# Kernel tuning notes

Measured on AMD Instinct MI355X. Metric: run time of the kernel, lower is better.

Reference implementation:

```python
import jax, jax.numpy as jnp
import numpy as np

N_HEADS = 8  # SD UNet default for hidden_size=1280
ADAPTER_SCALE = 1.0  # self.scale in SSRAttnProcessor


def setup_inputs() -> dict:
    key = jax.random.key(0)
    ks = jax.random.split(key, 7)
    B, S, D = 16, 4096, 1280
    T, C = 77, 768
    return {
        "hidden_states": jax.random.normal(ks[0], (B, S, D), jnp.float32),
        "encoder_hidden_states": jax.random.normal(ks[1], (B, T, C), jnp.float32),
        "w_q": jax.random.normal(ks[2], (D, D), jnp.float32) * (D ** -0.5),
        "w_k_ssr": jax.random.normal(ks[3], (D, C), jnp.float32) * (C ** -0.5),
        "w_v_ssr": jax.random.normal(ks[4], (D, C), jnp.float32) * (C ** -0.5),
        "w_out": jax.random.normal(ks[5], (D, D), jnp.float32) * (D ** -0.5),
        "b_out": jnp.zeros((D,), jnp.float32),
    }


def reference(hidden_states, encoder_hidden_states, w_q, w_k_ssr, w_v_ssr, w_out, b_out):
    B, S, D = hidden_states.shape
    T = encoder_hidden_states.shape[1]
    H = N_HEADS
    d = D // H
    # projections (torch Linear: x @ W^T)
    q = jnp.einsum('bsc,dc->bsd', hidden_states, w_q)
    k = jnp.einsum('btc,dc->btd', encoder_hidden_states, w_k_ssr)
    v = jnp.einsum('btc,dc->btd', encoder_hidden_states, w_v_ssr)
    # head split: [B, H, S, d]
    q = q.reshape(B, S, H, d).transpose(0, 2, 1, 3)
    k = k.reshape(B, T, H, d).transpose(0, 2, 1, 3)
    v = v.reshape(B, T, H, d).transpose(0, 2, 1, 3)
    # attn.get_attention_scores: softmax(Q K^T * d^-0.5)
    scores = jnp.einsum('bhsd,bhtd->bhst', q, k) * (d ** -0.5)
    probs = jax.nn.softmax(scores, axis=-1)
    out = jnp.einsum('bhst,bhtd->bhsd', probs, v)
    out = out.transpose(0, 2, 1, 3).reshape(B, S, D)
    out = ADAPTER_SCALE * out
    # to_out[0] linear (+ identity dropout); residual_connection=False, rescale=1
    out = jnp.einsum('bsd,ed->bse', out, w_out) + b_out
    return out
```

## Files before the change

### kernel.cpp

```cpp
#include <hip/hip_runtime.h>
#include <hip/hip_bf16.h>

typedef __bf16 bf16x8 __attribute__((ext_vector_type(8)));
typedef short  short8 __attribute__((ext_vector_type(8)));
typedef float  f32x4  __attribute__((ext_vector_type(4)));

__device__ __forceinline__ short f2bs(float f) {
  return __builtin_bit_cast(short, __float2bfloat16(f));
}

__device__ __forceinline__ bf16x8 ldfrag(const short* p) {
  return *reinterpret_cast<const bf16x8*>(p);
}

__global__ __launch_bounds__(256) void cast_f32_bf16(const float* __restrict__ in,
                                                     short* __restrict__ out, int n) {
  int i = (blockIdx.x * 256 + threadIdx.x) * 4;
  if (i < n) {
    float4 v = *reinterpret_cast<const float4*>(in + i);
    out[i + 0] = f2bs(v.x);
    out[i + 1] = f2bs(v.y);
    out[i + 2] = f2bs(v.z);
    out[i + 3] = f2bs(v.w);
  }
}

template <typename AT, typename OT, bool BIAS>
__global__ __launch_bounds__(256)
void gemm_bt(const AT* __restrict__ A, const short* __restrict__ B,
             const float* __restrict__ bias, OT* __restrict__ C,
             int M, int N, int K) {
  __shared__ short As[128][40];
  __shared__ short Bs[128][40];

  const int tid  = threadIdx.x;
  const int wave = tid >> 6, lane = tid & 63;
  const int quad = lane >> 4, l16 = lane & 15;
  const int wy = wave >> 1, wx = wave & 1;
  const int row0 = blockIdx.y * 128, col0 = blockIdx.x * 128;

  const int sr = tid >> 2;
  const int sc = (tid & 3) * 8;

  f32x4 acc[4][4] = {};

  for (int k0 = 0; k0 < K; k0 += 32) {
    for (int p = 0; p < 128; p += 64) {
      const int r  = sr + p;
      const int gm = row0 + r;
      short8 va = {0, 0, 0, 0, 0, 0, 0, 0};
      if (gm < M) {
        if constexpr (sizeof(AT) == 4) {
          const float* ap = (const float*)A + (size_t)gm * K + k0 + sc;
          float4 x = *reinterpret_cast<const float4*>(ap);
          float4 y = *reinterpret_cast<const float4*>(ap + 4);
          va[0] = f2bs(x.x); va[1] = f2bs(x.y); va[2] = f2bs(x.z); va[3] = f2bs(x.w);
          va[4] = f2bs(y.x); va[5] = f2bs(y.y); va[6] = f2bs(y.z); va[7] = f2bs(y.w);
        } else {
          va = *reinterpret_cast<const short8*>((const short*)A + (size_t)gm * K + k0 + sc);
        }
      }
      *reinterpret_cast<short8*>(&As[r][sc]) = va;
      *reinterpret_cast<short8*>(&Bs[r][sc]) =
          *reinterpret_cast<const short8*>(B + (size_t)(col0 + r) * K + k0 + sc);
    }
    __syncthreads();

    bf16x8 af[4], bfv[4];
#pragma unroll
    for (int i = 0; i < 4; i++) af[i]  = ldfrag(&As[wy * 64 + i * 16 + l16][quad * 8]);
#pragma unroll
    for (int i = 0; i < 4; i++) bfv[i] = ldfrag(&Bs[wx * 64 + i * 16 + l16][quad * 8]);
#pragma unroll
    for (int mi = 0; mi < 4; mi++)
#pragma unroll
      for (int ni = 0; ni < 4; ni++)
        acc[mi][ni] = __builtin_amdgcn_mfma_f32_16x16x32_bf16(af[mi], bfv[ni], acc[mi][ni], 0, 0, 0);
    __syncthreads();
  }

#pragma unroll
  for (int mi = 0; mi < 4; mi++) {
#pragma unroll
    for (int r = 0; r < 4; r++) {
      const int row = row0 + wy * 64 + mi * 16 + quad * 4 + r;
      if (row >= M) continue;
#pragma unroll
      for (int ni = 0; ni < 4; ni++) {
        const int col = col0 + wx * 64 + ni * 16 + l16;
        float v = acc[mi][ni][r];
        if constexpr (BIAS) v += bias[col];
        if constexpr (sizeof(OT) == 4)
          C[(size_t)row * N + col] = v;
        else
          C[(size_t)row * N + col] = f2bs(v);
      }
    }
  }
}

__global__ __launch_bounds__(256)
void attn_kernel(const short* __restrict__ Kp, const short* __restrict__ Vp,
                 short* __restrict__ Qb) {
  __shared__ short Vt[160][104];
  __shared__ short Pl[4][16][104];

  const int tid  = threadIdx.x;
  const int b = blockIdx.z, h = blockIdx.y, s0 = blockIdx.x * 64;
  const int wave = tid >> 6, lane = tid & 63;
  const int quad = lane >> 4, l16 = lane & 15;

  for (int idx = tid; idx < 77 * 160; idx += 256) {
    int t = idx / 160, i = idx - t * 160;
    Vt[i][t] = Vp[((size_t)(b * 77 + t)) * 1280 + h * 160 + i];
  }
  for (int idx = tid; idx < 160 * 19; idx += 256) {
    int i = idx / 19, t = 77 + (idx - i * 19);
    Vt[i][t] = 0;
  }
  __syncthreads();

  const short* Qg = Qb + ((size_t)b * 4096 + s0 + wave * 16 + l16) * 1280 + h * 160;
  bf16x8 qf[5];
#pragma unroll
  for (int kc = 0; kc < 5; kc++) qf[kc] = ldfrag(Qg + kc * 32 + quad * 8);

  f32x4 scv[5];
#pragma unroll
  for (int nt = 0; nt < 5; nt++) {
    f32x4 s = {};
    const short* Kg = Kp + ((size_t)(b * 77) + nt * 16 + l16) * 1280 + h * 160;
#pragma unroll
    for (int kc = 0; kc < 5; kc++) {
      bf16x8 kf = ldfrag(Kg + kc * 32 + quad * 8);
      s = __builtin_amdgcn_mfma_f32_16x16x32_bf16(qf[kc], kf, s, 0, 0, 0);
    }
    scv[nt] = s;
  }

  const float scale = 0.07905694150420949f;
#pragma unroll
  for (int r = 0; r < 4; r++) {
    float v[5];
    float m = -1e30f;
#pragma unroll
    for (int nt = 0; nt < 5; nt++) {
      v[nt] = scv[nt][r];
      if (nt * 16 + l16 < 77) m = fmaxf(m, v[nt]);
    }
#pragma unroll
    for (int off = 1; off < 16; off <<= 1) m = fmaxf(m, __shfl_xor(m, off));
    float sum = 0.f, p[5];
#pragma unroll
    for (int nt = 0; nt < 5; nt++) {
      p[nt] = (nt * 16 + l16 < 77) ? __expf((v[nt] - m) * scale) : 0.f;
      sum += p[nt];
    }
#pragma unroll
    for (int off = 1; off < 16; off <<= 1) sum += __shfl_xor(sum, off);
    const float inv = 1.f / sum;
    const int q = quad * 4 + r;
#pragma unroll
    for (int nt = 0; nt < 5; nt++) Pl[wave][q][nt * 16 + l16] = f2bs(p[nt] * inv);
    Pl[wave][q][80 + l16] = 0;
  }
  __syncthreads();

  bf16x8 pf[3];
#pragma unroll
  for (int kc = 0; kc < 3; kc++) pf[kc] = ldfrag(&Pl[wave][l16][kc * 32 + quad * 8]);

  short* Og = Qb + ((size_t)b * 4096 + s0 + wave * 16) * 1280 + h * 160;
#pragma unroll
  for (int nt = 0; nt < 10; nt++) {
    f32x4 o = {};
#pragma unroll
    for (int kc = 0; kc < 3; kc++) {
      bf16x8 vf = ldfrag(&Vt[nt * 16 + l16][kc * 32 + quad * 8]);
      o = __builtin_amdgcn_mfma_f32_16x16x32_bf16(pf[kc], vf, o, 0, 0, 0);
    }
#pragma unroll
    for (int r = 0; r < 4; r++) {
      const int q = quad * 4 + r;
      Og[(size_t)q * 1280 + nt * 16 + l16] = f2bs(o[r]);
    }
  }
}

extern "C" void kernel_launch(void* const* d_in, const int* in_sizes, int n_in,
                              void* d_out, int out_size, void* d_ws, size_t ws_size,
                              hipStream_t stream) {
  const float* hs  = (const float*)d_in[0];
  const float* enc = (const float*)d_in[1];
  const float* wq  = (const float*)d_in[2];
  const float* wk  = (const float*)d_in[3];
  const float* wv  = (const float*)d_in[4];
  const float* wo  = (const float*)d_in[5];
  const float* bo  = (const float*)d_in[6];
  float* out = (float*)d_out;

  char* ws = (char*)d_ws;
  short* wq_bf = (short*)(ws + 0);
  short* wk_bf = (short*)(ws + 3276800);
  short* wv_bf = (short*)(ws + 5242880);
  short* wo_bf = (short*)(ws + 7208960);
  short* Kp    = (short*)(ws + 10485760);
  short* Vp    = (short*)(ws + 13660160);
  short* Qb    = (short*)(ws + 16834560);
  if (ws_size < (size_t)184606720) return;

  cast_f32_bf16<<<1600, 256, 0, stream>>>(wq, wq_bf, 1638400);
  cast_f32_bf16<<<960,  256, 0, stream>>>(wk, wk_bf, 983040);
  cast_f32_bf16<<<960,  256, 0, stream>>>(wv, wv_bf, 983040);
  cast_f32_bf16<<<1600, 256, 0, stream>>>(wo, wo_bf, 1638400);

  dim3 g_kv(10, 10);
  gemm_bt<float, short, false><<<g_kv, 256, 0, stream>>>(enc, wk_bf, nullptr, Kp, 1232, 1280, 768);
  gemm_bt<float, short, false><<<g_kv, 256, 0, stream>>>(enc, wv_bf, nullptr, Vp, 1232, 1280, 768);

  dim3 g_q(10, 512);
  gemm_bt<float, short, false><<<g_q, 256, 0, stream>>>(hs, wq_bf, nullptr, Qb, 65536, 1280, 1280);

  dim3 g_a(64, 8, 16);
  attn_kernel<<<g_a, 256, 0, stream>>>(Kp, Vp, Qb);

  gemm_bt<short, float, true><<<g_q, 256, 0, stream>>>(Qb, wo_bf, bo, out, 65536, 1280, 1280);
}
```

Measured before the change: 1.730 ms.

## Pre-cast activations to bf16 and stage GEMM tiles via direct global-to-LDS loads

Adds a separate pass that casts hidden_states to bf16, so the large Q and output projections can use a new GEMM that loads A and B tiles straight into LDS with global_load_lds, with no register round trip and no padding. Q is now stored temporarily in the output buffer, and the attention output goes to the bf16 activation buffer. The weight-cast kernel is widened to 8 elements per thread with vector stores. The trade is an extra full read and write of the 335 MB activation tensor, plus unpadded LDS rows that may cause bank conflicts.

```diff
diff --git a/kernel.cpp b/kernel.cpp
--- a/kernel.cpp
+++ b/kernel.cpp
@@ -13,23 +13,95 @@
   return *reinterpret_cast<const bf16x8*>(p);
 }
 
-__global__ __launch_bounds__(256) void cast_f32_bf16(const float* __restrict__ in,
-                                                     short* __restrict__ out, int n) {
-  int i = (blockIdx.x * 256 + threadIdx.x) * 4;
+__device__ __forceinline__ void gl2lds16(const short* g, short* lds_base) {
+  __builtin_amdgcn_global_load_lds(
+      (const __attribute__((address_space(1))) unsigned int*)g,
+      (__attribute__((address_space(3))) unsigned int*)lds_base, 16, 0, 0);
+}
+
+__global__ __launch_bounds__(256) void cast8_f32_bf16(const float* __restrict__ in,
+                                                      short* __restrict__ out, long n) {
+  long i = ((long)blockIdx.x * 256 + threadIdx.x) * 8;
   if (i < n) {
-    float4 v = *reinterpret_cast<const float4*>(in + i);
-    out[i + 0] = f2bs(v.x);
-    out[i + 1] = f2bs(v.y);
-    out[i + 2] = f2bs(v.z);
-    out[i + 3] = f2bs(v.w);
-  }
-}
-
-template <typename AT, typename OT, bool BIAS>
+    float4 a = *reinterpret_cast<const float4*>(in + i);
+    float4 b = *reinterpret_cast<const float4*>(in + i + 4);
+    short8 v;
+    v[0] = f2bs(a.x); v[1] = f2bs(a.y); v[2] = f2bs(a.z); v[3] = f2bs(a.w);
+    v[4] = f2bs(b.x); v[5] = f2bs(b.y); v[6] = f2bs(b.z); v[7] = f2bs(b.w);
+    *reinterpret_cast<short8*>(out + i) = v;
+  }
+}
+
+template <typename OT, bool BIAS>
 __global__ __launch_bounds__(256)
-void gemm_bt(const AT* __restrict__ A, const short* __restrict__ B,
-             const float* __restrict__ bias, OT* __restrict__ C,
-             int M, int N, int K) {
+void gemm_fast(const short* __restrict__ A, const short* __restrict__ B,
+               const float* __restrict__ bias, OT* __restrict__ C,
+               int M, int N, int K) {
+  __shared__ short As[128 * 32];
+  __shared__ short Bs[128 * 32];
+
+  const int tid  = threadIdx.x;
+  const int wave = tid >> 6, lane = tid & 63;
+  const int quad = lane >> 4, l16 = lane & 15;
+  const int wy = wave >> 1, wx = wave & 1;
+  const size_t row0 = (size_t)blockIdx.y * 128, col0 = (size_t)blockIdx.x * 128;
+
+  const int srow = lane >> 2;
+  const int scol = (lane & 3) * 8;
+
+  const short* Ab0 = A + (row0 + wave * 32 + srow) * (size_t)K + scol;
+  const short* Ab1 = Ab0 + (size_t)16 * K;
+  const short* Bb0 = B + (col0 + wave * 32 + srow) * (size_t)K + scol;
+  const short* Bb1 = Bb0 + (size_t)16 * K;
+  short* const Al0 = &As[(wave * 32) * 32];
+  short* const Al1 = &As[(wave * 32 + 16) * 32];
+  short* const Bl0 = &Bs[(wave * 32) * 32];
+  short* const Bl1 = &Bs[(wave * 32 + 16) * 32];
+
+  f32x4 acc[4][4] = {};
+
+  for (int k0 = 0; k0 < K; k0 += 32) {
+    gl2lds16(Ab0 + k0, Al0);
+    gl2lds16(Ab1 + k0, Al1);
+    gl2lds16(Bb0 + k0, Bl0);
+    gl2lds16(Bb1 + k0, Bl1);
+    __syncthreads();
+
+    bf16x8 af[4], bv[4];
+#pragma unroll
+    for (int i = 0; i < 4; i++) af[i] = ldfrag(&As[(wy * 64 + i * 16 + l16) * 32 + quad * 8]);
+#pragma unroll
+    for (int i = 0; i < 4; i++) bv[i] = ldfrag(&Bs[(wx * 64 + i * 16 + l16) * 32 + quad * 8]);
+#pragma unroll
+    for (int mi = 0; mi < 4; mi++)
+#pragma unroll
+      for (int ni = 0; ni < 4; ni++)
+        acc[mi][ni] = __builtin_amdgcn_mfma_f32_16x16x32_bf16(af[mi], bv[ni], acc[mi][ni], 0, 0, 0);
+    __syncthreads();
+  }
+
+#pragma unroll
+  for (int mi = 0; mi < 4; mi++) {
+#pragma unroll
+    for (int r = 0; r < 4; r++) {
+      const size_t row = row0 + wy * 64 + mi * 16 + quad * 4 + r;
+#pragma unroll
+      for (int ni = 0; ni < 4; ni++) {
+        const size_t col = col0 + wx * 64 + ni * 16 + l16;
+        float v = acc[mi][ni][r];
+        if constexpr (BIAS) v += bias[col];
+        if constexpr (sizeof(OT) == 4)
+          C[row * N + col] = v;
+        else
+          C[row * N + col] = f2bs(v);
+      }
+    }
+  }
+}
+
+__global__ __launch_bounds__(256)
+void gemm_small(const float* __restrict__ A, const short* __restrict__ B,
+                short* __restrict__ C, int M, int N, int K) {
   __shared__ short As[128][40];
   __shared__ short Bs[128][40];
 
@@ -38,7 +110,6 @@
   const int quad = lane >> 4, l16 = lane & 15;
   const int wy = wave >> 1, wx = wave & 1;
   const int row0 = blockIdx.y * 128, col0 = blockIdx.x * 128;
-
   const int sr = tid >> 2;
   const int sc = (tid & 3) * 8;
 
@@ -50,15 +121,11 @@
       const int gm = row0 + r;
       short8 va = {0, 0, 0, 0, 0, 0, 0, 0};
       if (gm < M) {
-        if constexpr (sizeof(AT) == 4) {
-          const float* ap = (const float*)A + (size_t)gm * K + k0 + sc;
-          float4 x = *reinterpret_cast<const float4*>(ap);
-          float4 y = *reinterpret_cast<const float4*>(ap + 4);
-          va[0] = f2bs(x.x); va[1] = f2bs(x.y); va[2] = f2bs(x.z); va[3] = f2bs(x.w);
-          va[4] = f2bs(y.x); va[5] = f2bs(y.y); va[6] = f2bs(y.z); va[7] = f2bs(y.w);
-        } else {
-          va = *reinterpret_cast<const short8*>((const short*)A + (size_t)gm * K + k0 + sc);
-        }
+        const float* ap = A + (size_t)gm * K + k0 + sc;
+        float4 x = *reinterpret_cast<const float4*>(ap);
+        float4 y = *reinterpret_cast<const float4*>(ap + 4);
+        va[0] = f2bs(x.x); va[1] = f2bs(x.y); va[2] = f2bs(x.z); va[3] = f2bs(x.w);
+        va[4] = f2bs(y.x); va[5] = f2bs(y.y); va[6] = f2bs(y.z); va[7] = f2bs(y.w);
       }
       *reinterpret_cast<short8*>(&As[r][sc]) = va;
       *reinterpret_cast<short8*>(&Bs[r][sc]) =
@@ -66,16 +133,16 @@
     }
     __syncthreads();
 
-    bf16x8 af[4], bfv[4];
-#pragma unroll
-    for (int i = 0; i < 4; i++) af[i]  = ldfrag(&As[wy * 64 + i * 16 + l16][quad * 8]);
-#pragma unroll
-    for (int i = 0; i < 4; i++) bfv[i] = ldfrag(&Bs[wx * 64 + i * 16 + l16][quad * 8]);
+    bf16x8 af[4], bv[4];
+#pragma unroll
+    for (int i = 0; i < 4; i++) af[i] = ldfrag(&As[wy * 64 + i * 16 + l16][quad * 8]);
+#pragma unroll
+    for (int i = 0; i < 4; i++) bv[i] = ldfrag(&Bs[wx * 64 + i * 16 + l16][quad * 8]);
 #pragma unroll
     for (int mi = 0; mi < 4; mi++)
 #pragma unroll
       for (int ni = 0; ni < 4; ni++)
-        acc[mi][ni] = __builtin_amdgcn_mfma_f32_16x16x32_bf16(af[mi], bfv[ni], acc[mi][ni], 0, 0, 0);
+        acc[mi][ni] = __builtin_amdgcn_mfma_f32_16x16x32_bf16(af[mi], bv[ni], acc[mi][ni], 0, 0, 0);
     __syncthreads();
   }
 
@@ -88,12 +155,7 @@
 #pragma unroll
       for (int ni = 0; ni < 4; ni++) {
         const int col = col0 + wx * 64 + ni * 16 + l16;
-        float v = acc[mi][ni][r];
-        if constexpr (BIAS) v += bias[col];
-        if constexpr (sizeof(OT) == 4)
-          C[(size_t)row * N + col] = v;
-        else
-          C[(size_t)row * N + col] = f2bs(v);
+        C[(size_t)row * N + col] = f2bs(acc[mi][ni][r]);
       }
     }
   }
@@ -101,7 +163,7 @@
 
 __global__ __launch_bounds__(256)
 void attn_kernel(const short* __restrict__ Kp, const short* __restrict__ Vp,
-                 short* __restrict__ Qb) {
+                 const short* __restrict__ Qin, short* __restrict__ Oout) {
   __shared__ short Vt[160][104];
   __shared__ short Pl[4][16][104];
 
@@ -120,7 +182,7 @@
   }
   __syncthreads();
 
-  const short* Qg = Qb + ((size_t)b * 4096 + s0 + wave * 16 + l16) * 1280 + h * 160;
+  const short* Qg = Qin + ((size_t)b * 4096 + s0 + wave * 16 + l16) * 1280 + h * 160;
   bf16x8 qf[5];
 #pragma unroll
   for (int kc = 0; kc < 5; kc++) qf[kc] = ldfrag(Qg + kc * 32 + quad * 8);
@@ -170,7 +232,7 @@
 #pragma unroll
   for (int kc = 0; kc < 3; kc++) pf[kc] = ldfrag(&Pl[wave][l16][kc * 32 + quad * 8]);
 
-  short* Og = Qb + ((size_t)b * 4096 + s0 + wave * 16) * 1280 + h * 160;
+  short* Og = Oout + ((size_t)b * 4096 + s0 + wave * 16) * 1280 + h * 160;
 #pragma unroll
   for (int nt = 0; nt < 10; nt++) {
     f32x4 o = {};
@@ -206,23 +268,26 @@
   short* wo_bf = (short*)(ws + 7208960);
   short* Kp    = (short*)(ws + 10485760);
   short* Vp    = (short*)(ws + 13660160);
-  short* Qb    = (short*)(ws + 16834560);
+  short* Xbf   = (short*)(ws + 16834560);
   if (ws_size < (size_t)184606720) return;
 
-  cast_f32_bf16<<<1600, 256, 0, stream>>>(wq, wq_bf, 1638400);
-  cast_f32_bf16<<<960,  256, 0, stream>>>(wk, wk_bf, 983040);
-  cast_f32_bf16<<<960,  256, 0, stream>>>(wv, wv_bf, 983040);
-  cast_f32_bf16<<<1600, 256, 0, stream>>>(wo, wo_bf, 1638400);
+  short* Qb = (short*)d_out;
+
+  cast8_f32_bf16<<<800, 256, 0, stream>>>(wq, wq_bf, 1638400);
+  cast8_f32_bf16<<<480, 256, 0, stream>>>(wk, wk_bf, 983040);
+  cast8_f32_bf16<<<480, 256, 0, stream>>>(wv, wv_bf, 983040);
+  cast8_f32_bf16<<<800, 256, 0, stream>>>(wo, wo_bf, 1638400);
+  cast8_f32_bf16<<<40960, 256, 0, stream>>>(hs, Xbf, 83886080);
 
   dim3 g_kv(10, 10);
-  gemm_bt<float, short, false><<<g_kv, 256, 0, stream>>>(enc, wk_bf, nullptr, Kp, 1232, 1280, 768);
-  gemm_bt<float, short, false><<<g_kv, 256, 0, stream>>>(enc, wv_bf, nullptr, Vp, 1232, 1280, 768);
+  gemm_small<<<g_kv, 256, 0, stream>>>(enc, wk_bf, Kp, 1232, 1280, 768);
+  gemm_small<<<g_kv, 256, 0, stream>>>(enc, wv_bf, Vp, 1232, 1280, 768);
 
   dim3 g_q(10, 512);
-  gemm_bt<float, short, false><<<g_q, 256, 0, stream>>>(hs, wq_bf, nullptr, Qb, 65536, 1280, 1280);
+  gemm_fast<short, false><<<g_q, 256, 0, stream>>>(Xbf, wq_bf, nullptr, Qb, 65536, 1280, 1280);
 
   dim3 g_a(64, 8, 16);
-  attn_kernel<<<g_a, 256, 0, stream>>>(Kp, Vp, Qb);
-
-  gemm_bt<short, float, true><<<g_q, 256, 0, stream>>>(Qb, wo_bf, bo, out, 65536, 1280, 1280);
-}
+  attn_kernel<<<g_a, 256, 0, stream>>>(Kp, Vp, Qb, Xbf);
+
+  gemm_fast<float, true><<<g_q, 256, 0, stream>>>(Xbf, wo_bf, bo, out, 65536, 1280, 1280);
+}
```

New measurement: 1.534 ms. 11.4% less time.
